# Performance work log

Measured on AMD Instinct MI355X. Metric: run time of the kernel, lower is better.

Reference implementation:

```python
import jax, jax.numpy as jnp
import numpy as np

B, S, D = 4, 2048, 768
H, DH = 12, 64  # num heads, head dim


def setup_inputs() -> dict:
    key = jax.random.key(0)
    ks = jax.random.split(key, 4)
    scale = 0.02
    return {
        "hidden_states": jax.random.normal(ks[0], (B, S, D), dtype=jnp.float32),
        "attention_mask": jnp.zeros((B, 1, 1, S), dtype=jnp.float32),
        "Wq": jax.random.normal(ks[1], (D, D), dtype=jnp.float32) * scale,
        "bq": jnp.zeros((D,), dtype=jnp.float32),
        "Wk": jax.random.normal(ks[2], (D, D), dtype=jnp.float32) * scale,
        "bk": jnp.zeros((D,), dtype=jnp.float32),
        "Wv": jax.random.normal(ks[3], (D, D), dtype=jnp.float32) * scale,
        "bv": jnp.zeros((D,), dtype=jnp.float32),
    }


def _split_heads(x):
    # [B, S, D] -> [B, H, S, DH]
    b, s, _ = x.shape
    return x.reshape(b, s, H, DH).transpose(0, 2, 1, 3)


def reference(hidden_states, attention_mask, Wq, bq, Wk, bk, Wv, bv):
    q = _split_heads(hidden_states @ Wq.T + bq)
    k = _split_heads(hidden_states @ Wk.T + bk)
    v = _split_heads(hidden_states @ Wv.T + bv)
    # scores: [B, H, S, S]
    scores = jnp.einsum("bhqd,bhkd->bhqk", q, k) / jnp.sqrt(jnp.float32(DH))
    scores = scores + attention_mask
    probs = jax.nn.softmax(scores, axis=-1)
    # dropout prob = 0.0 (eval) -> identity
    ctx = jnp.einsum("bhqk,bhkd->bhqd", probs, v)
    ctx = ctx.transpose(0, 2, 1, 3).reshape(hidden_states.shape[0], hidden_states.shape[1], D)
    return ctx
```

## Files before the change

kernel.cpp:

```cpp
#include <hip/hip_runtime.h>

#define S_LEN 2048
#define DMODEL 768
#define NH 12
#define DHEAD 64
#define BATCH 4
#define MROWS (BATCH * S_LEN)
#define NQK 1536
#define LOG2E 1.44269504088896340736f

using short8 = __attribute__((ext_vector_type(8))) short;
using f32x4  = __attribute__((ext_vector_type(4))) float;
using f32x16 = __attribute__((ext_vector_type(16))) float;

typedef const __attribute__((address_space(1))) void* gas_ptr;
typedef __attribute__((address_space(3))) void* las_ptr;

__device__ __forceinline__ void gl2lds16(const void* g, void* l) {
  __builtin_amdgcn_global_load_lds((gas_ptr)(unsigned long long)g,
                                   (las_ptr)(unsigned int)(unsigned long long)l,
                                   16, 0, 0);
}

__device__ inline unsigned short f2bf(float f) {
  union { float f; unsigned int u; } c; c.f = f;
  unsigned int u = c.u;
  unsigned int r = (u + 0x7FFFu + ((u >> 16) & 1u)) >> 16;
  return (unsigned short)r;
}

__device__ inline unsigned int pack2bf(float a, float b) {
  union { float f; unsigned int u; } ca, cb;
  ca.f = a; cb.f = b;
  unsigned int ua = ca.u, ub = cb.u;
  ua = (ua + 0x7FFFu + ((ua >> 16) & 1u)) >> 16;
  ub = (ub + 0x7FFFu + ((ub >> 16) & 1u)) & 0xFFFF0000u;
  return ua | ub;
}

__global__ __launch_bounds__(256) void prep_kernel(
    const float* __restrict__ hs, const float* __restrict__ Wq,
    const float* __restrict__ Wk, const float* __restrict__ Wv,
    const float* __restrict__ mask,
    unsigned short* __restrict__ Xb, unsigned short* __restrict__ Wall,
    float* __restrict__ mask2)
{
  const int NX = MROWS * DMODEL / 4;
  const int NW = DMODEL * DMODEL / 4;
  const int NM = (BATCH * S_LEN) / 4;
  int i = blockIdx.x * 256 + threadIdx.x;
  if (i < NX) {
    float4 f = ((const float4*)hs)[i];
    ushort4 o = { f2bf(f.x), f2bf(f.y), f2bf(f.z), f2bf(f.w) };
    ((ushort4*)Xb)[i] = o;
  } else if (i < NX + 3 * NW) {
    int j = i - NX;
    int sec = j / NW, r = j - sec * NW;
    const float* src = (sec == 0) ? Wq : (sec == 1) ? Wk : Wv;
    float4 f = ((const float4*)src)[r];
    ushort4 o = { f2bf(f.x), f2bf(f.y), f2bf(f.z), f2bf(f.w) };
    ((ushort4*)(Wall + (size_t)sec * DMODEL * DMODEL))[r] = o;
  } else if (i < NX + 3 * NW + NM) {
    int r = i - NX - 3 * NW;
    float4 m = ((const float4*)mask)[r];
    float4 o = { (m.x - 10.f) * LOG2E, (m.y - 10.f) * LOG2E,
                 (m.z - 10.f) * LOG2E, (m.w - 10.f) * LOG2E };
    ((float4*)mask2)[r] = o;
  }
}

__global__ __launch_bounds__(256) void qkv_gemm(
    const unsigned short* __restrict__ Xb,
    const unsigned short* __restrict__ Wall,
    const float* __restrict__ bq,
    const float* __restrict__ bk,
    const float* __restrict__ bv,
    unsigned short* __restrict__ OutQK,
    unsigned short* __restrict__ Vt)
{
  __shared__ __align__(16) short As[128][64];
  __shared__ __align__(16) short Bs[128][64];

  int m0 = blockIdx.y * 128;
  int n0 = blockIdx.x * 128;
  int t = threadIdx.x;
  int w = t >> 6, lane = t & 63, lg = lane >> 4, lc = lane & 15;
  int wr = (w >> 1) * 64, wc = (w & 1) * 64;

  int srow = lane >> 3;
  int schunk = (lane & 7) ^ srow;

  f32x4 acc[4][4] = {};

  for (int k0 = 0; k0 < DMODEL; k0 += 64) {
    __syncthreads();
    for (int it = 0; it < 4; ++it) {
      int rb = w * 32 + it * 8;
      int r = rb + srow;
      gl2lds16(&Xb[(size_t)(m0 + r) * DMODEL + k0 + schunk * 8], &As[rb][0]);
      gl2lds16(&Wall[(size_t)(n0 + r) * DMODEL + k0 + schunk * 8], &Bs[rb][0]);
    }
    __syncthreads();
    for (int ks = 0; ks < 2; ++ks) {
      short8 a[4], b[4];
      for (int mt = 0; mt < 4; ++mt)
        a[mt] = *(const short8*)&As[wr + mt * 16 + lc][(((ks * 4 + lg) ^ (lc & 7))) * 8];
      for (int nt = 0; nt < 4; ++nt)
        b[nt] = *(const short8*)&Bs[wc + nt * 16 + lc][(((ks * 4 + lg) ^ (lc & 7))) * 8];
      for (int mt = 0; mt < 4; ++mt)
        for (int nt = 0; nt < 4; ++nt)
          acc[mt][nt] = __builtin_amdgcn_mfma_f32_16x16x32_bf16(a[mt], b[nt], acc[mt][nt], 0, 0, 0);
    }
  }

  if (n0 < NQK) {
    for (int nt = 0; nt < 4; ++nt) {
      int col = n0 + wc + nt * 16 + lc;
      float bb = (col < 768) ? bq[col] : bk[col - 768];
      float sc = (col < 768) ? (0.125f * LOG2E) : 1.0f;
      for (int mt = 0; mt < 4; ++mt) {
        int row = m0 + wr + mt * 16 + lg * 4;
        for (int i = 0; i < 4; ++i)
          OutQK[(size_t)(row + i) * NQK + col] = f2bf((acc[mt][nt][i] + bb) * sc);
      }
    }
  } else {
    int lgs = ((lg & 1) << 1) | (lg >> 1);
    int b = m0 >> 11;
    int sb0 = (m0 & 2047) + wr;
    for (int nt = 0; nt < 4; ++nt) {
      int hd = n0 + wc + nt * 16 + lc - NQK;
      int h = hd >> 6, d = hd & 63;
      float bb = bv[hd];
      size_t obase = ((size_t)((b * NH + h) * DHEAD + d)) * S_LEN;
      for (int mt = 0; mt < 4; ++mt) {
        int sb = sb0 + mt * 16 + lgs * 4;
        uint2 u;
        u.x = pack2bf(acc[mt][nt][0] + bb, acc[mt][nt][1] + bb);
        u.y = pack2bf(acc[mt][nt][2] + bb, acc[mt][nt][3] + bb);
        *(uint2*)&Vt[obase + sb] = u;
      }
    }
  }
}

__global__ __launch_bounds__(256, 3) void flash_attn(
    const unsigned short* __restrict__ QK,
    const unsigned short* __restrict__ Vt,
    const float* __restrict__ mask2,
    float* __restrict__ out)
{
  int qt = blockIdx.x, h = blockIdx.y, b = blockIdx.z;
  __shared__ __align__(16) short Ks0[64][64], Vs0[64][64];
  __shared__ __align__(16) short Ks1[64][64], Vs1[64][64];

  int t = threadIdx.x, w = t >> 6, lane = t & 63;
  int m31 = lane & 31, hf = lane >> 5;
  int q0 = qt * 128;
  int srow = lane >> 3;
  int schunk = (lane & 7) ^ srow;

  size_t vtbase = (size_t)((b * NH + h) * DHEAD) * S_LEN;
  const float* mrow = mask2 + (size_t)b * S_LEN;
  size_t kbase0 = (size_t)(b * S_LEN) * NQK + 768 + h * DHEAD;

  short8 qf[4];
  {
    size_t qrow = (size_t)(b * S_LEN + q0 + w * 32 + m31) * NQK + h * DHEAD;
    for (int kk = 0; kk < 4; ++kk)
      qf[kk] = *(const short8*)&QK[qrow + kk * 16 + hf * 8];
  }

  float lsum = 0.f;
  f32x16 o[2] = {};

  int rb0 = w * 16, rb1 = w * 16 + 8;
  int r0 = rb0 + srow, r1 = rb1 + srow;

  gl2lds16(&QK[kbase0 + (size_t)r0 * NQK + schunk * 8], &Ks0[rb0][0]);
  gl2lds16(&QK[kbase0 + (size_t)r1 * NQK + schunk * 8], &Ks0[rb1][0]);
  gl2lds16(&Vt[vtbase + (size_t)r0 * S_LEN + schunk * 8], &Vs0[rb0][0]);
  gl2lds16(&Vt[vtbase + (size_t)r1 * S_LEN + schunk * 8], &Vs0[rb1][0]);

  auto body = [&](auto& Kc, auto& Vc, auto& Kn, auto& Vn, int kt) {
    int k0 = kt * 64;
    __syncthreads();

    if (kt + 1 < S_LEN / 64) {
      int k1 = k0 + 64;
      gl2lds16(&QK[kbase0 + (size_t)(k1 + r0) * NQK + schunk * 8], &Kn[rb0][0]);
      gl2lds16(&QK[kbase0 + (size_t)(k1 + r1) * NQK + schunk * 8], &Kn[rb1][0]);
      gl2lds16(&Vt[vtbase + (size_t)r0 * S_LEN + k1 + schunk * 8], &Vn[rb0][0]);
      gl2lds16(&Vt[vtbase + (size_t)r1 * S_LEN + k1 + schunk * 8], &Vn[rb1][0]);
    }

    f32x16 s[2] = {};
    for (int kk = 0; kk < 4; ++kk)
      for (int mt = 0; mt < 2; ++mt) {
        int r = mt * 32 + m31;
        short8 ak = *(const short8*)&Kc[r][((kk * 2 + hf) ^ (r & 7)) * 8];
        s[mt] = __builtin_amdgcn_mfma_f32_32x32x16_bf16(ak, qf[kk], s[mt], 0, 0, 0);
      }

    unsigned int pk[16];
    for (int mt = 0; mt < 2; ++mt)
      for (int g = 0; g < 4; ++g) {
        float4 mv = *(const float4*)&mrow[k0 + mt * 32 + g * 8 + hf * 4];
        float p0 = exp2f(s[mt][g * 4 + 0] + mv.x);
        float p1 = exp2f(s[mt][g * 4 + 1] + mv.y);
        float p2 = exp2f(s[mt][g * 4 + 2] + mv.z);
        float p3 = exp2f(s[mt][g * 4 + 3] + mv.w);
        lsum += (p0 + p1) + (p2 + p3);
        pk[mt * 8 + g * 2 + 0] = pack2bf(p0, p1);
        pk[mt * 8 + g * 2 + 1] = pack2bf(p2, p3);
      }

    for (int kk = 0; kk < 4; ++kk) {
      union { unsigned int u[4]; short8 s8; } af;
      af.u[0] = pk[kk * 4 + 0]; af.u[1] = pk[kk * 4 + 1];
      af.u[2] = pk[kk * 4 + 2]; af.u[3] = pk[kk * 4 + 3];
      for (int nt = 0; nt < 2; ++nt) {
        int r = nt * 32 + m31;
        short8 bv = *(const short8*)&Vc[r][((kk * 2 + hf) ^ (r & 7)) * 8];
        o[nt] = __builtin_amdgcn_mfma_f32_32x32x16_bf16(af.s8, bv, o[nt], 0, 0, 0);
      }
    }
  };

  for (int kt = 0; kt < S_LEN / 64; kt += 2) {
    body(Ks0, Vs0, Ks1, Vs1, kt);
    body(Ks1, Vs1, Ks0, Vs0, kt + 1);
  }

  lsum += __shfl_xor(lsum, 32, 64);
  float inv = 1.0f / lsum;
  float lv[16];
  for (int r = 0; r < 16; ++r)
    lv[r] = __shfl(inv, (r & 3) + 8 * (r >> 2) + 4 * hf, 64);

  for (int nt = 0; nt < 2; ++nt)
    for (int r = 0; r < 16; ++r) {
      int qrow = (r & 3) + 8 * (r >> 2) + 4 * hf;
      int q = q0 + w * 32 + qrow;
      out[(size_t)(b * S_LEN + q) * DMODEL + h * DHEAD + nt * 32 + m31] = o[nt][r] * lv[r];
    }
}

extern "C" void kernel_launch(void* const* d_in, const int* in_sizes, int n_in,
                              void* d_out, int out_size, void* d_ws, size_t ws_size,
                              hipStream_t stream) {
  const float* hs   = (const float*)d_in[0];
  const float* mask = (const float*)d_in[1];
  const float* Wq   = (const float*)d_in[2];
  const float* bq   = (const float*)d_in[3];
  const float* Wk   = (const float*)d_in[4];
  const float* bk   = (const float*)d_in[5];
  const float* Wv   = (const float*)d_in[6];
  const float* bv   = (const float*)d_in[7];
  float* out = (float*)d_out;

  char* ws = (char*)d_ws;
  const size_t XB_BYTES   = (size_t)MROWS * DMODEL * 2;
  const size_t QK_BYTES   = (size_t)MROWS * NQK * 2;
  const size_t VT_BYTES   = (size_t)MROWS * DMODEL * 2;
  const size_t WALL_BYTES = (size_t)3 * DMODEL * DMODEL * 2;
  unsigned short* Xb    = (unsigned short*)ws;
  unsigned short* QK    = (unsigned short*)(ws + XB_BYTES);
  unsigned short* Vtg   = (unsigned short*)(ws + XB_BYTES + QK_BYTES);
  unsigned short* Wall  = (unsigned short*)(ws + XB_BYTES + QK_BYTES + VT_BYTES);
  float*          mask2 = (float*)(ws + XB_BYTES + QK_BYTES + VT_BYTES + WALL_BYTES);

  const int NX = MROWS * DMODEL / 4;
  const int NW = DMODEL * DMODEL / 4;
  const int NM = (BATCH * S_LEN) / 4;
  int nprep = NX + 3 * NW + NM;
  prep_kernel<<<(nprep + 255) / 256, 256, 0, stream>>>(hs, Wq, Wk, Wv, mask, Xb, Wall, mask2);

  qkv_gemm<<<dim3(2304 / 128, MROWS / 128), 256, 0, stream>>>(Xb, Wall, bq, bk, bv, QK, Vtg);

  flash_attn<<<dim3(S_LEN / 128, NH, BATCH), 256, 0, stream>>>(QK, Vtg, mask2, out);
}
```

Baseline: 239.9 us.

## Remap grids to XCD-aware 1D order and drop flash-attn double buffering

Both kernels now launch a 1D grid. Block IDs are remapped so that blocks landing on the same XCD (id & 7) work on neighbouring M-tiles or the same batch/head group, which is meant to improve L2 reuse of shared K/V and weight tiles. The flash attention kernel also drops its double-buffered LDS prefetch in favour of a single buffer with load-then-sync each iteration, and removes the occupancy hint of 3. This halves LDS use and may raise occupancy, but it gives up the overlap of global loads with MFMA work.

After: 242.3 us. No clear change (+1.0%).

```diff
diff --git a/kernel.cpp b/kernel.cpp
--- a/kernel.cpp
+++ b/kernel.cpp
@@ -81,8 +81,11 @@
   __shared__ __align__(16) short As[128][64];
   __shared__ __align__(16) short Bs[128][64];
 
-  int m0 = blockIdx.y * 128;
-  int n0 = blockIdx.x * 128;
+  int id = blockIdx.x;
+  int xcd = id & 7, slot = id >> 3;
+  int m0 = (xcd * 8 + slot / 18) * 128;
+  int n0 = (slot % 18) * 128;
+
   int t = threadIdx.x;
   int w = t >> 6, lane = t & 63, lg = lane >> 4, lc = lane & 15;
   int wr = (w >> 1) * 64, wc = (w & 1) * 64;
@@ -144,15 +147,20 @@
   }
 }
 
-__global__ __launch_bounds__(256, 3) void flash_attn(
+__global__ __launch_bounds__(256) void flash_attn(
     const unsigned short* __restrict__ QK,
     const unsigned short* __restrict__ Vt,
     const float* __restrict__ mask2,
     float* __restrict__ out)
 {
-  int qt = blockIdx.x, h = blockIdx.y, b = blockIdx.z;
-  __shared__ __align__(16) short Ks0[64][64], Vs0[64][64];
-  __shared__ __align__(16) short Ks1[64][64], Vs1[64][64];
+  int id = blockIdx.x;
+  int xcd = id & 7, slot = id >> 3;
+  int grp = xcd * 6 + (slot >> 4);
+  int qt = slot & 15;
+  int b = grp / NH, h = grp % NH;
+
+  __shared__ __align__(16) short Ks[64][64];
+  __shared__ __align__(16) short Vs[64][64];
 
   int t = threadIdx.x, w = t >> 6, lane = t & 63;
   int m31 = lane & 31, hf = lane >> 5;
@@ -177,28 +185,20 @@
   int rb0 = w * 16, rb1 = w * 16 + 8;
   int r0 = rb0 + srow, r1 = rb1 + srow;
 
-  gl2lds16(&QK[kbase0 + (size_t)r0 * NQK + schunk * 8], &Ks0[rb0][0]);
-  gl2lds16(&QK[kbase0 + (size_t)r1 * NQK + schunk * 8], &Ks0[rb1][0]);
-  gl2lds16(&Vt[vtbase + (size_t)r0 * S_LEN + schunk * 8], &Vs0[rb0][0]);
-  gl2lds16(&Vt[vtbase + (size_t)r1 * S_LEN + schunk * 8], &Vs0[rb1][0]);
-
-  auto body = [&](auto& Kc, auto& Vc, auto& Kn, auto& Vn, int kt) {
+  for (int kt = 0; kt < S_LEN / 64; ++kt) {
     int k0 = kt * 64;
     __syncthreads();
-
-    if (kt + 1 < S_LEN / 64) {
-      int k1 = k0 + 64;
-      gl2lds16(&QK[kbase0 + (size_t)(k1 + r0) * NQK + schunk * 8], &Kn[rb0][0]);
-      gl2lds16(&QK[kbase0 + (size_t)(k1 + r1) * NQK + schunk * 8], &Kn[rb1][0]);
-      gl2lds16(&Vt[vtbase + (size_t)r0 * S_LEN + k1 + schunk * 8], &Vn[rb0][0]);
-      gl2lds16(&Vt[vtbase + (size_t)r1 * S_LEN + k1 + schunk * 8], &Vn[rb1][0]);
-    }
+    gl2lds16(&QK[kbase0 + (size_t)(k0 + r0) * NQK + schunk * 8], &Ks[rb0][0]);
+    gl2lds16(&QK[kbase0 + (size_t)(k0 + r1) * NQK + schunk * 8], &Ks[rb1][0]);
+    gl2lds16(&Vt[vtbase + (size_t)r0 * S_LEN + k0 + schunk * 8], &Vs[rb0][0]);
+    gl2lds16(&Vt[vtbase + (size_t)r1 * S_LEN + k0 + schunk * 8], &Vs[rb1][0]);
+    __syncthreads();
 
     f32x16 s[2] = {};
     for (int kk = 0; kk < 4; ++kk)
       for (int mt = 0; mt < 2; ++mt) {
         int r = mt * 32 + m31;
-        short8 ak = *(const short8*)&Kc[r][((kk * 2 + hf) ^ (r & 7)) * 8];
+        short8 ak = *(const short8*)&Ks[r][((kk * 2 + hf) ^ (r & 7)) * 8];
         s[mt] = __builtin_amdgcn_mfma_f32_32x32x16_bf16(ak, qf[kk], s[mt], 0, 0, 0);
       }
 
@@ -221,15 +221,10 @@
       af.u[2] = pk[kk * 4 + 2]; af.u[3] = pk[kk * 4 + 3];
       for (int nt = 0; nt < 2; ++nt) {
         int r = nt * 32 + m31;
-        short8 bv = *(const short8*)&Vc[r][((kk * 2 + hf) ^ (r & 7)) * 8];
+        short8 bv = *(const short8*)&Vs[r][((kk * 2 + hf) ^ (r & 7)) * 8];
         o[nt] = __builtin_amdgcn_mfma_f32_32x32x16_bf16(af.s8, bv, o[nt], 0, 0, 0);
       }
     }
-  };
-
-  for (int kt = 0; kt < S_LEN / 64; kt += 2) {
-    body(Ks0, Vs0, Ks1, Vs1, kt);
-    body(Ks1, Vs1, Ks0, Vs0, kt + 1);
   }
 
   lsum += __shfl_xor(lsum, 32, 64);
@@ -276,7 +271,7 @@
   int nprep = NX + 3 * NW + NM;
   prep_kernel<<<(nprep + 255) / 256, 256, 0, stream>>>(hs, Wq, Wk, Wv, mask, Xb, Wall, mask2);
 
-  qkv_gemm<<<dim3(2304 / 128, MROWS / 128), 256, 0, stream>>>(Xb, Wall, bq, bk, bv, QK, Vtg);
-
-  flash_attn<<<dim3(S_LEN / 128, NH, BATCH), 256, 0, stream>>>(QK, Vtg, mask2, out);
-}
+  qkv_gemm<<<1152, 256, 0, stream>>>(Xb, Wall, bq, bk, bv, QK, Vtg);
+
+  flash_attn<<<768, 256, 0, stream>>>(QK, Vtg, mask2, out);
+}
```
